# Performance work log

Hardware: AMD Instinct MI355X
Metric: run time of the kernel (lower is better)

The kernel has to match this reference:

```python
import jax, jax.numpy as jnp
import numpy as np
import math

B, T, C = 32768, 32, 32  # seq len and embed dim are pinned to 32 by the source code


def setup_inputs() -> dict:
    key = jax.random.key(0)
    ks = jax.random.split(key, 9)
    s = 1.0 / math.sqrt(C)
    x = jax.random.normal(ks[0], (B, T, C), jnp.float32)
    Wk = jax.random.normal(ks[1], (C, C), jnp.float32) * s
    bk = jax.random.normal(ks[2], (C,), jnp.float32) * s
    Wq = jax.random.normal(ks[3], (C, C), jnp.float32) * s
    bq = jax.random.normal(ks[4], (C,), jnp.float32) * s
    Wv = jax.random.normal(ks[5], (C, C), jnp.float32) * s
    bv = jax.random.normal(ks[6], (C,), jnp.float32) * s
    Wp = jax.random.normal(ks[7], (C, C), jnp.float32) * s
    bp = jax.random.normal(ks[8], (C,), jnp.float32) * s
    return {"x": x, "Wk": Wk, "bk": bk, "Wq": Wq, "bq": bq,
            "Wv": Wv, "bv": bv, "Wp": Wp, "bp": bp}


def reference(x, Wk, bk, Wq, bq, Wv, bv, Wp, bp):
    # torch Linear: y = x @ W^T + b
    k = x @ Wk.T + bk          # [B, T, C]
    q = x @ Wq.T + bq
    v = x @ Wv.T + bv
    # att = q k^T / sqrt(C)  -> [B, T, T]
    att = jnp.matmul(q, jnp.swapaxes(k, -2, -1)) / math.sqrt(C)
    # mask is [1,1,T,T]; out-of-place masked_fill broadcasts att to [1,B,T,T]
    mask = jnp.tril(jnp.ones((T, T), jnp.float32))[None, None]  # [1,1,T,T]
    att = jnp.where(mask == 0, -jnp.inf, att[None])             # [1,B,T,T]
    att = jax.nn.softmax(att, axis=-1)
    # y = att @ v^T : [1,B,T,T] @ [B,C,T] -> [1,B,T,T]  (valid because C == T)
    y = jnp.matmul(att, jnp.swapaxes(v, -2, -1))
    # transpose(1,2) then view(B, -1, C) -- faithful permutation + reshape
    y = jnp.transpose(y, (0, 2, 1, 3)).reshape(B, -1, C)        # [B, T, C]
    return y @ Wp.T + bp
```

## Files before the change

### kernel.cpp

```cpp
#include <hip/hip_runtime.h>

typedef __bf16 bf16x8 __attribute__((ext_vector_type(8)));
typedef float  f32x16 __attribute__((ext_vector_type(16)));
typedef unsigned int uint4v __attribute__((ext_vector_type(4)));

#define MFMA32(A, B, C) __builtin_amdgcn_mfma_f32_32x32x16_bf16((A), (B), (C), 0, 0, 0)

__device__ __forceinline__ bf16x8 load8_bf(const float* __restrict__ p, float scale) {
    const float4 a = *reinterpret_cast<const float4*>(p);
    const float4 b = *reinterpret_cast<const float4*>(p + 4);
    bf16x8 r;
    r[0] = (__bf16)(a.x * scale); r[1] = (__bf16)(a.y * scale);
    r[2] = (__bf16)(a.z * scale); r[3] = (__bf16)(a.w * scale);
    r[4] = (__bf16)(b.x * scale); r[5] = (__bf16)(b.y * scale);
    r[6] = (__bf16)(b.z * scale); r[7] = (__bf16)(b.w * scale);
    return r;
}

__device__ __forceinline__ unsigned pack2(float a, float b) {
    unsigned la = (unsigned)__builtin_bit_cast(unsigned short, (__bf16)a);
    unsigned lb = (unsigned)__builtin_bit_cast(unsigned short, (__bf16)b);
    return la | (lb << 16);
}

__device__ __forceinline__ void swap32(unsigned& a, unsigned& b) {
#if __has_builtin(__builtin_amdgcn_permlane32_swap)
    auto r = __builtin_amdgcn_permlane32_swap(a, b, false, false);
    a = r[0]; b = r[1];
#else
    asm("v_permlane32_swap_b32 %0, %1" : "+v"(a), "+v"(b));
#endif
}

__device__ __forceinline__ void rearrange(const f32x16& a, bf16x8& f0, bf16x8& f1) {
    unsigned D0 = pack2(a[0], a[1]),   D1 = pack2(a[2], a[3]);
    unsigned D2 = pack2(a[4], a[5]),   D3 = pack2(a[6], a[7]);
    unsigned D4 = pack2(a[8], a[9]),   D5 = pack2(a[10], a[11]);
    unsigned D6 = pack2(a[12], a[13]), D7 = pack2(a[14], a[15]);
    swap32(D0, D2); swap32(D1, D3); swap32(D4, D6); swap32(D5, D7);
    f0 = __builtin_bit_cast(bf16x8, uint4v{D0, D1, D2, D3});
    f1 = __builtin_bit_cast(bf16x8, uint4v{D4, D5, D6, D7});
}

__device__ __forceinline__ void ld4(const float* __restrict__ p,
                                    float4& r0, float4& r1, float4& r2, float4& r3) {
    r0 = *reinterpret_cast<const float4*>(p);
    r1 = *reinterpret_cast<const float4*>(p + 4);
    r2 = *reinterpret_cast<const float4*>(p + 16);
    r3 = *reinterpret_cast<const float4*>(p + 20);
}

__device__ __forceinline__ void cvt8(const float4& a, const float4& b, bf16x8& f) {
    f[0] = (__bf16)a.x; f[1] = (__bf16)a.y; f[2] = (__bf16)a.z; f[3] = (__bf16)a.w;
    f[4] = (__bf16)b.x; f[5] = (__bf16)b.y; f[6] = (__bf16)b.z; f[7] = (__bf16)b.w;
}

__global__ __launch_bounds__(256, 3) void attn32(
    const float* __restrict__ x,
    const float* __restrict__ Wk, const float* __restrict__ bk,
    const float* __restrict__ Wq, const float* __restrict__ bq,
    const float* __restrict__ Wv, const float* __restrict__ bv,
    const float* __restrict__ Wp, const float* __restrict__ bp,
    float* __restrict__ out, int Btot)
{
    const int lane = threadIdx.x & 63;
    const int col  = lane & 31;
    const int hi   = lane >> 5;

    const float SC = 0.17677669529663687f * 1.4426950408889634f;

    const int wrow = col * 32 + hi * 8;
    const bf16x8 wk0 = load8_bf(Wk + wrow, 1.f), wk1 = load8_bf(Wk + wrow + 16, 1.f);
    const bf16x8 wq0 = load8_bf(Wq + wrow, SC),  wq1 = load8_bf(Wq + wrow + 16, SC);
    const bf16x8 wv0 = load8_bf(Wv + wrow, 1.f), wv1 = load8_bf(Wv + wrow + 16, 1.f);
    const bf16x8 wp0 = load8_bf(Wp + wrow, 1.f), wp1 = load8_bf(Wp + wrow + 16, 1.f);

    f32x16 bk16, bq16, bv16;
#pragma unroll
    for (int e = 0; e < 16; ++e) {
        const int r = (e & 3) + 8 * (e >> 2) + 4 * hi;
        bk16[e] = bk[r];
        bq16[e] = bq[r] * SC;
        bv16[e] = bv[r];
    }
    const float bpv = bp[col];

    const int gw = blockIdx.x * 4 + (threadIdx.x >> 6);
    const int nw = gridDim.x * 4;

    float4 A0, A1, A2, A3;
    if (gw < Btot) ld4(x + (size_t)gw * 1024 + wrow, A0, A1, A2, A3);

    for (int b = gw; b < Btot; b += nw) {
        bf16x8 xa0, xa1;
        cvt8(A0, A1, xa0);
        cvt8(A2, A3, xa1);
        const int nb = b + nw;
        if (nb < Btot) ld4(x + (size_t)nb * 1024 + wrow, A0, A1, A2, A3);

        f32x16 acc;

        acc = bk16;
        acc = MFMA32(wk0, xa0, acc);
        acc = MFMA32(wk1, xa1, acc);
        bf16x8 ka0, ka1; rearrange(acc, ka0, ka1);

        acc = bq16;
        acc = MFMA32(wq0, xa0, acc);
        acc = MFMA32(wq1, xa1, acc);
        bf16x8 qb0, qb1; rearrange(acc, qb0, qb1);

        acc = bv16;
        acc = MFMA32(wv0, xa0, acc);
        acc = MFMA32(wv1, xa1, acc);
        bf16x8 vb0, vb1; rearrange(acc, vb0, vb1);

        f32x16 s;
#pragma unroll
        for (int e = 0; e < 16; ++e) s[e] = 0.f;
        s = MFMA32(ka0, qb0, s);
        s = MFMA32(ka1, qb1, s);

        float sv[16];
        float m = -3.0e38f;
#pragma unroll
        for (int e = 0; e < 16; ++e) {
            const int j = (e & 3) + 8 * (e >> 2) + 4 * hi;
            sv[e] = (j <= col) ? s[e] : -__builtin_inff();
            m = fmaxf(m, sv[e]);
        }
        m = fmaxf(m, __shfl_xor(m, 32));
        float pe[16];
        float sum = 0.f;
#pragma unroll
        for (int e = 0; e < 16; ++e) { pe[e] = __builtin_amdgcn_exp2f(sv[e] - m); sum += pe[e]; }
        sum += __shfl_xor(sum, 32);
        const float inv = __builtin_amdgcn_rcpf(sum);
        f32x16 pv;
#pragma unroll
        for (int e = 0; e < 16; ++e) pv[e] = pe[e] * inv;
        bf16x8 pa0, pa1; rearrange(pv, pa0, pa1);

        f32x16 yt;
#pragma unroll
        for (int e = 0; e < 16; ++e) yt[e] = 0.f;
        yt = MFMA32(vb0, pa0, yt);
        yt = MFMA32(vb1, pa1, yt);
        bf16x8 ya0, ya1; rearrange(yt, ya0, ya1);

        f32x16 o;
#pragma unroll
        for (int e = 0; e < 16; ++e) o[e] = bpv;
        o = MFMA32(ya0, wp0, o);
        o = MFMA32(ya1, wp1, o);

        float* ob = out + (size_t)b * 32 + col;
#pragma unroll
        for (int e = 0; e < 16; ++e) {
            const int r = (e & 3) + 8 * (e >> 2) + 4 * hi;
            __builtin_nontemporal_store(o[e], ob + ((size_t)r << 20));
        }
    }
}

extern "C" void kernel_launch(void* const* d_in, const int* in_sizes, int n_in,
                              void* d_out, int out_size, void* d_ws, size_t ws_size,
                              hipStream_t stream) {
    const float* x  = (const float*)d_in[0];
    const float* Wk = (const float*)d_in[1];
    const float* bk = (const float*)d_in[2];
    const float* Wq = (const float*)d_in[3];
    const float* bq = (const float*)d_in[4];
    const float* Wv = (const float*)d_in[5];
    const float* bv = (const float*)d_in[6];
    const float* Wp = (const float*)d_in[7];
    const float* bp = (const float*)d_in[8];
    float* out = (float*)d_out;

    const int Btot = in_sizes[0] / 1024;
    dim3 grid(2048), block(256);
    hipLaunchKernelGGL(attn32, grid, block, 0, stream,
                       x, Wk, bk, Wq, bq, Wv, bv, Wp, bp, out, Btot);
}
```

Baseline: 53.17 us.

## Process two batches per wave in a one-shot grid with XCD-aware block swizzle

Replaces the persistent grid-stride loop with a grid sized to cover all batches. Each wave handles two batch elements, interleaving their MFMA chains and softmax for more instruction-level parallelism. Block indices are swizzled across the 8 XCDs, and the occupancy hint in launch_bounds is removed. In exchange, every wave reloads and converts the weights and biases, and the paired batches raise register pressure.

```diff
diff --git a/kernel.cpp b/kernel.cpp
--- a/kernel.cpp
+++ b/kernel.cpp
@@ -55,7 +55,7 @@
     f[4] = (__bf16)b.x; f[5] = (__bf16)b.y; f[6] = (__bf16)b.z; f[7] = (__bf16)b.w;
 }
 
-__global__ __launch_bounds__(256, 3) void attn32(
+__global__ __launch_bounds__(256) void attn32(
     const float* __restrict__ x,
     const float* __restrict__ Wk, const float* __restrict__ bk,
     const float* __restrict__ Wq, const float* __restrict__ bq,
@@ -67,9 +67,22 @@
     const int col  = lane & 31;
     const int hi   = lane >> 5;
 
+    const unsigned g = blockIdx.x;
+    const unsigned swz = (g & 7) * (gridDim.x >> 3) + (g >> 3);
+    const int pairIdx = (int)swz * 4 + (threadIdx.x >> 6);
+    const int bA = pairIdx * 2;
+    if (bA >= Btot) return;
+    const int bB = bA + 1;
+    const bool hasB = bB < Btot;
+
+    const int wrow = col * 32 + hi * 8;
+
+    float4 A0, A1, A2, A3, B0, B1, B2, B3;
+    ld4(x + (size_t)bA * 1024 + wrow, A0, A1, A2, A3);
+    ld4(x + (size_t)(hasB ? bB : bA) * 1024 + wrow, B0, B1, B2, B3);
+
     const float SC = 0.17677669529663687f * 1.4426950408889634f;
 
-    const int wrow = col * 32 + hi * 8;
     const bf16x8 wk0 = load8_bf(Wk + wrow, 1.f), wk1 = load8_bf(Wk + wrow + 16, 1.f);
     const bf16x8 wq0 = load8_bf(Wq + wrow, SC),  wq1 = load8_bf(Wq + wrow + 16, SC);
     const bf16x8 wv0 = load8_bf(Wv + wrow, 1.f), wv1 = load8_bf(Wv + wrow + 16, 1.f);
@@ -85,80 +98,94 @@
     }
     const float bpv = bp[col];
 
-    const int gw = blockIdx.x * 4 + (threadIdx.x >> 6);
-    const int nw = gridDim.x * 4;
-
-    float4 A0, A1, A2, A3;
-    if (gw < Btot) ld4(x + (size_t)gw * 1024 + wrow, A0, A1, A2, A3);
-
-    for (int b = gw; b < Btot; b += nw) {
-        bf16x8 xa0, xa1;
-        cvt8(A0, A1, xa0);
-        cvt8(A2, A3, xa1);
-        const int nb = b + nw;
-        if (nb < Btot) ld4(x + (size_t)nb * 1024 + wrow, A0, A1, A2, A3);
-
-        f32x16 acc;
-
-        acc = bk16;
-        acc = MFMA32(wk0, xa0, acc);
-        acc = MFMA32(wk1, xa1, acc);
-        bf16x8 ka0, ka1; rearrange(acc, ka0, ka1);
-
-        acc = bq16;
-        acc = MFMA32(wq0, xa0, acc);
-        acc = MFMA32(wq1, xa1, acc);
-        bf16x8 qb0, qb1; rearrange(acc, qb0, qb1);
-
-        acc = bv16;
-        acc = MFMA32(wv0, xa0, acc);
-        acc = MFMA32(wv1, xa1, acc);
-        bf16x8 vb0, vb1; rearrange(acc, vb0, vb1);
-
-        f32x16 s;
-#pragma unroll
-        for (int e = 0; e < 16; ++e) s[e] = 0.f;
-        s = MFMA32(ka0, qb0, s);
-        s = MFMA32(ka1, qb1, s);
-
-        float sv[16];
-        float m = -3.0e38f;
+    bf16x8 xaA0, xaA1, xaB0, xaB1;
+    cvt8(A0, A1, xaA0); cvt8(A2, A3, xaA1);
+    cvt8(B0, B1, xaB0); cvt8(B2, B3, xaB1);
+
+    f32x16 acc;
+
+    acc = bk16; acc = MFMA32(wk0, xaA0, acc); acc = MFMA32(wk1, xaA1, acc);
+    bf16x8 kaA0, kaA1; rearrange(acc, kaA0, kaA1);
+    acc = bk16; acc = MFMA32(wk0, xaB0, acc); acc = MFMA32(wk1, xaB1, acc);
+    bf16x8 kaB0, kaB1; rearrange(acc, kaB0, kaB1);
+
+    acc = bq16; acc = MFMA32(wq0, xaA0, acc); acc = MFMA32(wq1, xaA1, acc);
+    bf16x8 qbA0, qbA1; rearrange(acc, qbA0, qbA1);
+    acc = bq16; acc = MFMA32(wq0, xaB0, acc); acc = MFMA32(wq1, xaB1, acc);
+    bf16x8 qbB0, qbB1; rearrange(acc, qbB0, qbB1);
+
+    f32x16 sA, sB;
+#pragma unroll
+    for (int e = 0; e < 16; ++e) { sA[e] = 0.f; sB[e] = 0.f; }
+    sA = MFMA32(kaA0, qbA0, sA); sA = MFMA32(kaA1, qbA1, sA);
+    sB = MFMA32(kaB0, qbB0, sB); sB = MFMA32(kaB1, qbB1, sB);
+
+    acc = bv16; acc = MFMA32(wv0, xaA0, acc); acc = MFMA32(wv1, xaA1, acc);
+    bf16x8 vbA0, vbA1; rearrange(acc, vbA0, vbA1);
+    acc = bv16; acc = MFMA32(wv0, xaB0, acc); acc = MFMA32(wv1, xaB1, acc);
+    bf16x8 vbB0, vbB1; rearrange(acc, vbB0, vbB1);
+
+    f32x16 pvA, pvB;
+    {
+        float svA[16], svB[16];
+        float mA = -3.0e38f, mB = -3.0e38f;
 #pragma unroll
         for (int e = 0; e < 16; ++e) {
             const int j = (e & 3) + 8 * (e >> 2) + 4 * hi;
-            sv[e] = (j <= col) ? s[e] : -__builtin_inff();
-            m = fmaxf(m, sv[e]);
-        }
-        m = fmaxf(m, __shfl_xor(m, 32));
-        float pe[16];
-        float sum = 0.f;
-#pragma unroll
-        for (int e = 0; e < 16; ++e) { pe[e] = __builtin_amdgcn_exp2f(sv[e] - m); sum += pe[e]; }
-        sum += __shfl_xor(sum, 32);
-        const float inv = __builtin_amdgcn_rcpf(sum);
-        f32x16 pv;
-#pragma unroll
-        for (int e = 0; e < 16; ++e) pv[e] = pe[e] * inv;
-        bf16x8 pa0, pa1; rearrange(pv, pa0, pa1);
-
-        f32x16 yt;
-#pragma unroll
-        for (int e = 0; e < 16; ++e) yt[e] = 0.f;
-        yt = MFMA32(vb0, pa0, yt);
-        yt = MFMA32(vb1, pa1, yt);
-        bf16x8 ya0, ya1; rearrange(yt, ya0, ya1);
-
-        f32x16 o;
-#pragma unroll
-        for (int e = 0; e < 16; ++e) o[e] = bpv;
-        o = MFMA32(ya0, wp0, o);
-        o = MFMA32(ya1, wp1, o);
-
-        float* ob = out + (size_t)b * 32 + col;
+            svA[e] = (j <= col) ? sA[e] : -__builtin_inff();
+            svB[e] = (j <= col) ? sB[e] : -__builtin_inff();
+            mA = fmaxf(mA, svA[e]);
+            mB = fmaxf(mB, svB[e]);
+        }
+        mA = fmaxf(mA, __shfl_xor(mA, 32));
+        mB = fmaxf(mB, __shfl_xor(mB, 32));
+        float peA[16], peB[16];
+        float sumA = 0.f, sumB = 0.f;
+#pragma unroll
+        for (int e = 0; e < 16; ++e) {
+            peA[e] = __builtin_amdgcn_exp2f(svA[e] - mA); sumA += peA[e];
+            peB[e] = __builtin_amdgcn_exp2f(svB[e] - mB); sumB += peB[e];
+        }
+        sumA += __shfl_xor(sumA, 32);
+        sumB += __shfl_xor(sumB, 32);
+        const float invA = __builtin_amdgcn_rcpf(sumA);
+        const float invB = __builtin_amdgcn_rcpf(sumB);
+#pragma unroll
+        for (int e = 0; e < 16; ++e) { pvA[e] = peA[e] * invA; pvB[e] = peB[e] * invB; }
+    }
+    bf16x8 paA0, paA1, paB0, paB1;
+    rearrange(pvA, paA0, paA1);
+    rearrange(pvB, paB0, paB1);
+
+    f32x16 ytA, ytB;
+#pragma unroll
+    for (int e = 0; e < 16; ++e) { ytA[e] = 0.f; ytB[e] = 0.f; }
+    ytA = MFMA32(vbA0, paA0, ytA); ytA = MFMA32(vbA1, paA1, ytA);
+    ytB = MFMA32(vbB0, paB0, ytB); ytB = MFMA32(vbB1, paB1, ytB);
+    bf16x8 yaA0, yaA1, yaB0, yaB1;
+    rearrange(ytA, yaA0, yaA1);
+    rearrange(ytB, yaB0, yaB1);
+
+    f32x16 oA, oB;
+#pragma unroll
+    for (int e = 0; e < 16; ++e) { oA[e] = bpv; oB[e] = bpv; }
+    oA = MFMA32(yaA0, wp0, oA); oA = MFMA32(yaA1, wp1, oA);
+    oB = MFMA32(yaB0, wp0, oB); oB = MFMA32(yaB1, wp1, oB);
+
+    {
+        float* const ob = out + (size_t)bA * 32 + col;
 #pragma unroll
         for (int e = 0; e < 16; ++e) {
             const int r = (e & 3) + 8 * (e >> 2) + 4 * hi;
-            __builtin_nontemporal_store(o[e], ob + ((size_t)r << 20));
+            __builtin_nontemporal_store(oA[e], ob + ((size_t)r << 20));
+        }
+    }
+    if (hasB) {
+        float* const ob = out + (size_t)bB * 32 + col;
+#pragma unroll
+        for (int e = 0; e < 16; ++e) {
+            const int r = (e & 3) + 8 * (e >> 2) + 4 * hi;
+            __builtin_nontemporal_store(oB[e], ob + ((size_t)r << 20));
         }
     }
 }
@@ -178,7 +205,10 @@
     float* out = (float*)d_out;
 
     const int Btot = in_sizes[0] / 1024;
-    dim3 grid(2048), block(256);
+    const int pairs = (Btot + 1) / 2;
+    int blocks = (pairs + 3) / 4;
+    blocks = (blocks + 7) & ~7;
+    dim3 grid(blocks), block(256);
     hipLaunchKernelGGL(attn32, grid, block, 0, stream,
                        x, Wk, bk, Wq, bq, Wv, bv, Wp, bp, out, Btot);
 }
```

Result: slower. 70.34 us (+32.3%).

## Stage x tiles through LDS with async double-buffered global_load_lds

Applied to the files above, without the earlier changes.

Replaces register prefetch of the next x tile with asynchronous global-to-LDS loads into a per-wave double buffer, using an XOR swizzle so the later LDS reads avoid bank conflicts. A manual vmcnt wait keeps the prefetch outstanding while the output stores drain. The V projection is moved after the QK score MFMA, and the grid is resized so each wave handles about four batches. Launch bounds are relaxed. The manual waitcnt accounting is fragile, and LDS use may lower occupancy.

```diff
diff --git a/kernel.cpp b/kernel.cpp
--- a/kernel.cpp
+++ b/kernel.cpp
@@ -42,20 +42,23 @@
     f1 = __builtin_bit_cast(bf16x8, uint4v{D4, D5, D6, D7});
 }
 
-__device__ __forceinline__ void ld4(const float* __restrict__ p,
-                                    float4& r0, float4& r1, float4& r2, float4& r3) {
-    r0 = *reinterpret_cast<const float4*>(p);
-    r1 = *reinterpret_cast<const float4*>(p + 4);
-    r2 = *reinterpret_cast<const float4*>(p + 16);
-    r3 = *reinterpret_cast<const float4*>(p + 20);
-}
-
 __device__ __forceinline__ void cvt8(const float4& a, const float4& b, bf16x8& f) {
     f[0] = (__bf16)a.x; f[1] = (__bf16)a.y; f[2] = (__bf16)a.z; f[3] = (__bf16)a.w;
     f[4] = (__bf16)b.x; f[5] = (__bf16)b.y; f[6] = (__bf16)b.z; f[7] = (__bf16)b.w;
 }
 
-__global__ __launch_bounds__(256, 3) void attn32(
+__device__ __forceinline__ void stage_x(const char* __restrict__ xb, char* lslice,
+                                        const int* src_off) {
+#pragma unroll
+    for (int t = 0; t < 4; ++t) {
+        __builtin_amdgcn_global_load_lds(
+            (const __attribute__((address_space(1))) unsigned*)(xb + src_off[t]),
+            (__attribute__((address_space(3))) unsigned*)(lslice + t * 1024),
+            16, 0, 0);
+    }
+}
+
+__global__ __launch_bounds__(256) void attn32(
     const float* __restrict__ x,
     const float* __restrict__ Wk, const float* __restrict__ bk,
     const float* __restrict__ Wq, const float* __restrict__ bq,
@@ -63,9 +66,29 @@
     const float* __restrict__ Wp, const float* __restrict__ bp,
     float* __restrict__ out, int Btot)
 {
+    __shared__ char ldsx[4][2][4096];
+
     const int lane = threadIdx.x & 63;
     const int col  = lane & 31;
     const int hi   = lane >> 5;
+    const int wave = threadIdx.x >> 6;
+
+    const int gw = blockIdx.x * 4 + wave;
+    const int nw = gridDim.x * 4;
+    if (gw >= Btot) return;
+
+    char* const buf0 = &ldsx[wave][0][0];
+    char* const buf1 = &ldsx[wave][1][0];
+
+    int src_off[4];
+#pragma unroll
+    for (int t = 0; t < 4; ++t) {
+        const int A = t * 1024 + lane * 16;
+        src_off[t] = A ^ (((A >> 9) & 7) << 4);
+    }
+    const int W0 = col * 128 + hi * 32;
+    const int sw = ((W0 >> 9) & 7) << 4;
+    const int s0 = W0 ^ sw, s1 = (W0 + 16) ^ sw, s2 = (W0 + 64) ^ sw, s3 = (W0 + 80) ^ sw;
 
     const float SC = 0.17677669529663687f * 1.4426950408889634f;
 
@@ -85,35 +108,34 @@
     }
     const float bpv = bp[col];
 
-    const int gw = blockIdx.x * 4 + (threadIdx.x >> 6);
-    const int nw = gridDim.x * 4;
-
-    float4 A0, A1, A2, A3;
-    if (gw < Btot) ld4(x + (size_t)gw * 1024 + wrow, A0, A1, A2, A3);
-
-    for (int b = gw; b < Btot; b += nw) {
+    stage_x((const char*)(x + (size_t)gw * 1024), buf0, src_off);
+    asm volatile("s_waitcnt vmcnt(0)" ::: "memory");
+
+    bool parity = false;
+    for (int b = gw; b < Btot; b += nw, parity = !parity) {
+        const char* cur = parity ? buf1 : buf0;
+        char* nxt       = parity ? buf0 : buf1;
+
+        const int nb = b + nw;
+        if (nb < Btot)
+            stage_x((const char*)(x + (size_t)nb * 1024), nxt, src_off);
+        asm volatile("" ::: "memory");
+
+        const float4 A0 = *reinterpret_cast<const float4*>(cur + s0);
+        const float4 A1 = *reinterpret_cast<const float4*>(cur + s1);
+        const float4 A2 = *reinterpret_cast<const float4*>(cur + s2);
+        const float4 A3 = *reinterpret_cast<const float4*>(cur + s3);
         bf16x8 xa0, xa1;
         cvt8(A0, A1, xa0);
         cvt8(A2, A3, xa1);
-        const int nb = b + nw;
-        if (nb < Btot) ld4(x + (size_t)nb * 1024 + wrow, A0, A1, A2, A3);
 
         f32x16 acc;
 
-        acc = bk16;
-        acc = MFMA32(wk0, xa0, acc);
-        acc = MFMA32(wk1, xa1, acc);
+        acc = bk16; acc = MFMA32(wk0, xa0, acc); acc = MFMA32(wk1, xa1, acc);
         bf16x8 ka0, ka1; rearrange(acc, ka0, ka1);
 
-        acc = bq16;
-        acc = MFMA32(wq0, xa0, acc);
-        acc = MFMA32(wq1, xa1, acc);
+        acc = bq16; acc = MFMA32(wq0, xa0, acc); acc = MFMA32(wq1, xa1, acc);
         bf16x8 qb0, qb1; rearrange(acc, qb0, qb1);
-
-        acc = bv16;
-        acc = MFMA32(wv0, xa0, acc);
-        acc = MFMA32(wv1, xa1, acc);
-        bf16x8 vb0, vb1; rearrange(acc, vb0, vb1);
 
         f32x16 s;
 #pragma unroll
@@ -121,24 +143,29 @@
         s = MFMA32(ka0, qb0, s);
         s = MFMA32(ka1, qb1, s);
 
-        float sv[16];
-        float m = -3.0e38f;
-#pragma unroll
-        for (int e = 0; e < 16; ++e) {
-            const int j = (e & 3) + 8 * (e >> 2) + 4 * hi;
-            sv[e] = (j <= col) ? s[e] : -__builtin_inff();
-            m = fmaxf(m, sv[e]);
+        acc = bv16; acc = MFMA32(wv0, xa0, acc); acc = MFMA32(wv1, xa1, acc);
+        bf16x8 vb0, vb1; rearrange(acc, vb0, vb1);
+
+        f32x16 pv;
+        {
+            float sv[16];
+            float m = -3.0e38f;
+#pragma unroll
+            for (int e = 0; e < 16; ++e) {
+                const int j = (e & 3) + 8 * (e >> 2) + 4 * hi;
+                sv[e] = (j <= col) ? s[e] : -__builtin_inff();
+                m = fmaxf(m, sv[e]);
+            }
+            m = fmaxf(m, __shfl_xor(m, 32));
+            float pe[16];
+            float sum = 0.f;
+#pragma unroll
+            for (int e = 0; e < 16; ++e) { pe[e] = __builtin_amdgcn_exp2f(sv[e] - m); sum += pe[e]; }
+            sum += __shfl_xor(sum, 32);
+            const float inv = __builtin_amdgcn_rcpf(sum);
+#pragma unroll
+            for (int e = 0; e < 16; ++e) pv[e] = pe[e] * inv;
         }
-        m = fmaxf(m, __shfl_xor(m, 32));
-        float pe[16];
-        float sum = 0.f;
-#pragma unroll
-        for (int e = 0; e < 16; ++e) { pe[e] = __builtin_amdgcn_exp2f(sv[e] - m); sum += pe[e]; }
-        sum += __shfl_xor(sum, 32);
-        const float inv = __builtin_amdgcn_rcpf(sum);
-        f32x16 pv;
-#pragma unroll
-        for (int e = 0; e < 16; ++e) pv[e] = pe[e] * inv;
         bf16x8 pa0, pa1; rearrange(pv, pa0, pa1);
 
         f32x16 yt;
@@ -154,12 +181,17 @@
         o = MFMA32(ya0, wp0, o);
         o = MFMA32(ya1, wp1, o);
 
-        float* ob = out + (size_t)b * 32 + col;
+        asm volatile("" ::: "memory");
+
+        float* const ob = out + (size_t)b * 32 + col;
 #pragma unroll
         for (int e = 0; e < 16; ++e) {
             const int r = (e & 3) + 8 * (e >> 2) + 4 * hi;
             __builtin_nontemporal_store(o[e], ob + ((size_t)r << 20));
         }
+
+        asm volatile("s_waitcnt vmcnt(16)" ::: "memory");
+        __builtin_amdgcn_sched_barrier(0);
     }
 }
 
@@ -178,7 +210,9 @@
     float* out = (float*)d_out;
 
     const int Btot = in_sizes[0] / 1024;
-    dim3 grid(2048), block(256);
+    const int waves = (Btot + 3) / 4;
+    const int blocks = (waves + 3) / 4;
+    dim3 grid(blocks), block(256);
     hipLaunchKernelGGL(attn32, grid, block, 0, stream,
                        x, Wk, bk, Wq, bq, Wv, bv, Wp, bp, out, Btot);
 }
```

Result: slower. 58.43 us (+9.9%).

## Fold Wq^T Wk into one matrix and reassociate V with output projection

Applied to the files above, without the earlier changes.

Precomputes a combined scaled query-key weight matrix and a bias term per wave, so each score matrix is computed as x·(A·x^T + u) instead of separate K and Q projections. It drops the bk term, which is constant along each softmax row and cancels out. It also reassociates the value path, computing V·Wp first and then multiplying by the attention probabilities. This removes one projection's MFMAs and rearrange per batch. The cost is extra setup work per wave, strided column loads of the weights, and different bf16 rounding points that may change accuracy.

```diff
diff --git a/kernel.cpp b/kernel.cpp
--- a/kernel.cpp
+++ b/kernel.cpp
@@ -55,7 +55,7 @@
     f[4] = (__bf16)b.x; f[5] = (__bf16)b.y; f[6] = (__bf16)b.z; f[7] = (__bf16)b.w;
 }
 
-__global__ __launch_bounds__(256, 3) void attn32(
+__global__ __launch_bounds__(256) void attn32(
     const float* __restrict__ x,
     const float* __restrict__ Wk, const float* __restrict__ bk,
     const float* __restrict__ Wq, const float* __restrict__ bq,
@@ -67,29 +67,47 @@
     const int col  = lane & 31;
     const int hi   = lane >> 5;
 
+    const int gw = blockIdx.x * 4 + (threadIdx.x >> 6);
+    const int nw = gridDim.x * 4;
+    if (gw >= Btot) return;
+
     const float SC = 0.17677669529663687f * 1.4426950408889634f;
 
     const int wrow = col * 32 + hi * 8;
-    const bf16x8 wk0 = load8_bf(Wk + wrow, 1.f), wk1 = load8_bf(Wk + wrow + 16, 1.f);
-    const bf16x8 wq0 = load8_bf(Wq + wrow, SC),  wq1 = load8_bf(Wq + wrow + 16, SC);
+
+    float4 A0, A1, A2, A3;
+    ld4(x + (size_t)gw * 1024 + wrow, A0, A1, A2, A3);
+
     const bf16x8 wv0 = load8_bf(Wv + wrow, 1.f), wv1 = load8_bf(Wv + wrow + 16, 1.f);
     const bf16x8 wp0 = load8_bf(Wp + wrow, 1.f), wp1 = load8_bf(Wp + wrow + 16, 1.f);
 
-    f32x16 bk16, bq16, bv16;
+    bf16x8 wkc0, wkc1, wqc0, wqc1, bqb0, bqb1;
 #pragma unroll
-    for (int e = 0; e < 16; ++e) {
-        const int r = (e & 3) + 8 * (e >> 2) + 4 * hi;
-        bk16[e] = bk[r];
-        bq16[e] = bq[r] * SC;
-        bv16[e] = bv[r];
+    for (int q = 0; q < 8; ++q) {
+        wkc0[q] = (__bf16)Wk[(hi * 8 + q) * 32 + col];
+        wkc1[q] = (__bf16)Wk[(16 + hi * 8 + q) * 32 + col];
+        wqc0[q] = (__bf16)(SC * Wq[(hi * 8 + q) * 32 + col]);
+        wqc1[q] = (__bf16)(SC * Wq[(16 + hi * 8 + q) * 32 + col]);
+        bqb0[q] = (__bf16)(SC * bq[hi * 8 + q]);
+        bqb1[q] = (__bf16)(SC * bq[16 + hi * 8 + q]);
     }
+
+    f32x16 acc;
+#pragma unroll
+    for (int e = 0; e < 16; ++e) acc[e] = 0.f;
+
+    acc = MFMA32(wqc0, wkc0, acc);
+    acc = MFMA32(wqc1, wkc1, acc);
+    bf16x8 nA0, nA1; rearrange(acc, nA0, nA1);
+
+#pragma unroll
+    for (int e = 0; e < 16; ++e) acc[e] = 0.f;
+    acc = MFMA32(wkc0, bqb0, acc);
+    acc = MFMA32(wkc1, bqb1, acc);
+    const f32x16 u16 = acc;
+
+    const float bvv = bv[col];
     const float bpv = bp[col];
-
-    const int gw = blockIdx.x * 4 + (threadIdx.x >> 6);
-    const int nw = gridDim.x * 4;
-
-    float4 A0, A1, A2, A3;
-    if (gw < Btot) ld4(x + (size_t)gw * 1024 + wrow, A0, A1, A2, A3);
 
     for (int b = gw; b < Btot; b += nw) {
         bf16x8 xa0, xa1;
@@ -98,63 +116,58 @@
         const int nb = b + nw;
         if (nb < Btot) ld4(x + (size_t)nb * 1024 + wrow, A0, A1, A2, A3);
 
-        f32x16 acc;
+#pragma unroll
+        for (int e = 0; e < 16; ++e) acc[e] = bvv;
+        acc = MFMA32(xa0, wv0, acc);
+        acc = MFMA32(xa1, wv1, acc);
+        bf16x8 vT0, vT1; rearrange(acc, vT0, vT1);
 
-        acc = bk16;
-        acc = MFMA32(wk0, xa0, acc);
-        acc = MFMA32(wk1, xa1, acc);
-        bf16x8 ka0, ka1; rearrange(acc, ka0, ka1);
+#pragma unroll
+        for (int e = 0; e < 16; ++e) acc[e] = 0.f;
+        acc = MFMA32(vT0, wp0, acc);
+        acc = MFMA32(vT1, wp1, acc);
+        bf16x8 rB0, rB1; rearrange(acc, rB0, rB1);
 
-        acc = bq16;
-        acc = MFMA32(wq0, xa0, acc);
-        acc = MFMA32(wq1, xa1, acc);
-        bf16x8 qb0, qb1; rearrange(acc, qb0, qb1);
-
-        acc = bv16;
-        acc = MFMA32(wv0, xa0, acc);
-        acc = MFMA32(wv1, xa1, acc);
-        bf16x8 vb0, vb1; rearrange(acc, vb0, vb1);
+        acc = u16;
+        acc = MFMA32(nA0, xa0, acc);
+        acc = MFMA32(nA1, xa1, acc);
+        bf16x8 hb0, hb1; rearrange(acc, hb0, hb1);
 
         f32x16 s;
 #pragma unroll
         for (int e = 0; e < 16; ++e) s[e] = 0.f;
-        s = MFMA32(ka0, qb0, s);
-        s = MFMA32(ka1, qb1, s);
+        s = MFMA32(xa0, hb0, s);
+        s = MFMA32(xa1, hb1, s);
 
-        float sv[16];
-        float m = -3.0e38f;
+        f32x16 pv;
+        {
+            float sv[16];
+            float m = -3.0e38f;
 #pragma unroll
-        for (int e = 0; e < 16; ++e) {
-            const int j = (e & 3) + 8 * (e >> 2) + 4 * hi;
-            sv[e] = (j <= col) ? s[e] : -__builtin_inff();
-            m = fmaxf(m, sv[e]);
+            for (int e = 0; e < 16; ++e) {
+                const int j = (e & 3) + 8 * (e >> 2) + 4 * hi;
+                sv[e] = (j <= col) ? s[e] : -__builtin_inff();
+                m = fmaxf(m, sv[e]);
+            }
+            m = fmaxf(m, __shfl_xor(m, 32));
+            float pe[16];
+            float sum = 0.f;
+#pragma unroll
+            for (int e = 0; e < 16; ++e) { pe[e] = __builtin_amdgcn_exp2f(sv[e] - m); sum += pe[e]; }
+            sum += __shfl_xor(sum, 32);
+            const float inv = __builtin_amdgcn_rcpf(sum);
+#pragma unroll
+            for (int e = 0; e < 16; ++e) pv[e] = pe[e] * inv;
         }
-        m = fmaxf(m, __shfl_xor(m, 32));
-        float pe[16];
-        float sum = 0.f;
-#pragma unroll
-        for (int e = 0; e < 16; ++e) { pe[e] = __builtin_amdgcn_exp2f(sv[e] - m); sum += pe[e]; }
-        sum += __shfl_xor(sum, 32);
-        const float inv = __builtin_amdgcn_rcpf(sum);
-        f32x16 pv;
-#pragma unroll
-        for (int e = 0; e < 16; ++e) pv[e] = pe[e] * inv;
         bf16x8 pa0, pa1; rearrange(pv, pa0, pa1);
-
-        f32x16 yt;
-#pragma unroll
-        for (int e = 0; e < 16; ++e) yt[e] = 0.f;
-        yt = MFMA32(vb0, pa0, yt);
-        yt = MFMA32(vb1, pa1, yt);
-        bf16x8 ya0, ya1; rearrange(yt, ya0, ya1);
 
         f32x16 o;
 #pragma unroll
         for (int e = 0; e < 16; ++e) o[e] = bpv;
-        o = MFMA32(ya0, wp0, o);
-        o = MFMA32(ya1, wp1, o);
+        o = MFMA32(pa0, rB0, o);
+        o = MFMA32(pa1, rB1, o);
 
-        float* ob = out + (size_t)b * 32 + col;
+        float* const ob = out + (size_t)b * 32 + col;
 #pragma unroll
         for (int e = 0; e < 16; ++e) {
             const int r = (e & 3) + 8 * (e >> 2) + 4 * hi;
```

New measurement: 51.46 us. 3.2% less time.
